# Performance work log

Hardware: AMD Instinct MI355X
Metric: run time of the kernel (lower is better)

Reference implementation:

```python
import jax, jax.numpy as jnp
import numpy as np

N_NODES = 50000
N_EDGES = 800000
DIM = 512
N_CLASSES = 1000


def _xavier(key, shape):
    fan_in, fan_out = shape[0], shape[1]
    lim = float(np.sqrt(6.0 / (fan_in + fan_out)))
    return jax.random.uniform(key, shape, jnp.float32, -lim, lim)


def setup_inputs() -> dict:
    key = jax.random.key(0)
    ks = jax.random.split(key, 12)
    nodes = jax.random.normal(ks[0], (N_NODES, DIM), jnp.float32)
    edges = jax.random.randint(ks[1], (2, N_EDGES), 0, N_NODES, jnp.int64)
    labelmatrix = jax.random.normal(ks[2], (N_CLASSES, 128), jnp.float32)
    return {
        "nodes": nodes,
        "edges": edges,
        "labelmatrix": labelmatrix,
        "W1": _xavier(ks[3], (DIM, 256)), "b1": jnp.zeros((256,), jnp.float32),
        "W2": _xavier(ks[4], (256, 192)), "b2": jnp.zeros((192,), jnp.float32),
        "W3": _xavier(ks[5], (192, 128)), "b3": jnp.zeros((128,), jnp.float32),
        "fc1_w": _xavier(ks[6], (128, 128)), "fc1_b": jnp.zeros((128,), jnp.float32),
        "fc2_w": _xavier(ks[7], (128, 128)), "fc2_b": jnp.zeros((128,), jnp.float32),
    }


def _gcn_conv(x, W, b, src, dst, n):
    # PyG GCNConv: add self-loops, symmetric normalization, then aggregate.
    xw = x @ W                                        # [N, out]
    ones = jnp.ones(src.shape[0], x.dtype)
    deg = jax.ops.segment_sum(ones, dst, num_segments=n) + 1.0  # +1 self-loop
    dinv = jax.lax.rsqrt(deg)                         # deg^{-1/2}
    coef = dinv[src] * dinv[dst]                      # [E]
    agg = jax.ops.segment_sum(xw[src] * coef[:, None], dst, num_segments=n)
    agg = agg + xw * (dinv * dinv)[:, None]           # self-loop contribution
    return agg + b


def reference(nodes, edges, labelmatrix, W1, b1, W2, b2, W3, b3,
              fc1_w, fc1_b, fc2_w, fc2_b):
    src, dst = edges[0], edges[1]
    n = nodes.shape[0]
    # _GraphConv: three stacked GCNConv layers, no inter-layer activation
    x = _gcn_conv(nodes, W1, b1, src, dst, n)
    x = _gcn_conv(x, W2, b2, src, dst, n)
    x = _gcn_conv(x, W3, b3, src, dst, n)             # [N, 128]
    # _GraphLinear (eval mode: dropout is identity)
    h = jax.nn.relu(x @ fc1_w + fc1_b)
    h = h @ fc2_w + fc2_b                             # [N, 128]
    preds = h @ labelmatrix.T                         # dot-product similarity [N, C]
    return preds
```

## Files before the change

kernel.cpp:

```cpp
#include <hip/hip_runtime.h>

typedef unsigned short u16;
typedef __bf16 bf16x8 __attribute__((ext_vector_type(8)));
typedef float f32x4 __attribute__((ext_vector_type(4)));

__device__ __forceinline__ u16 f2bf(float f) {
    unsigned int u = __float_as_uint(f);
    unsigned int r = (u + 0x7FFFu + ((u >> 16) & 1u)) >> 16;
    return (u16)r;
}
__device__ __forceinline__ float bf_lo(unsigned int u) { return __uint_as_float(u << 16); }
__device__ __forceinline__ float bf_hi(unsigned int u) { return __uint_as_float(u & 0xFFFF0000u); }

#define GLOAD_LDS(gp, lp) \
    __builtin_amdgcn_global_load_lds( \
        (const __attribute__((address_space(1))) unsigned int*)(gp), \
        (__attribute__((address_space(3))) unsigned int*)(lp), 16, 0, 0)


__global__ void hist_k(const int* __restrict__ dst, int* __restrict__ deg, int nE) {
    int e = blockIdx.x * 256 + threadIdx.x;
    if (e < nE) atomicAdd(&deg[dst[e]], 1);
}

__global__ void scan_block_k(const int* __restrict__ deg, int* __restrict__ scanned,
                             int* __restrict__ bsums, int n) {
    __shared__ int s[1024];
    int i = blockIdx.x * 1024 + threadIdx.x;
    int v = (i < n) ? deg[i] : 0;
    s[threadIdx.x] = v;
    __syncthreads();
    for (int off = 1; off < 1024; off <<= 1) {
        int t = (threadIdx.x >= off) ? s[threadIdx.x - off] : 0;
        __syncthreads();
        s[threadIdx.x] += t;
        __syncthreads();
    }
    if (i < n) scanned[i] = s[threadIdx.x];
    if (threadIdx.x == 1023) bsums[blockIdx.x] = s[1023];
}

__global__ void scan_sums_k(int* __restrict__ bsums, int nb) {
    int l = threadIdx.x & 63;
    int v = (l < nb) ? bsums[l] : 0;
    int orig = v;
    for (int off = 1; off < 64; off <<= 1) {
        int t = __shfl_up(v, off);
        if (l >= off) v += t;
    }
    if (l < nb) bsums[l] = v - orig;
}

__global__ void scan_final_dinv_k(const int* __restrict__ scanned, const int* __restrict__ deg,
                                  const int* __restrict__ bsums, int* __restrict__ rowptr,
                                  int* __restrict__ wptr, float* __restrict__ dinv,
                                  int n, int nE) {
    int i = blockIdx.x * 256 + threadIdx.x;
    if (i < n) {
        int rp = scanned[i] - deg[i] + bsums[i >> 10];
        rowptr[i] = rp;
        wptr[i] = rp;
        dinv[i] = rsqrtf((float)deg[i] + 1.0f);
    }
    if (i == 0) rowptr[n] = nE;
}

__global__ void csr_fill_k(const int* __restrict__ src, const int* __restrict__ dst,
                           int* __restrict__ wptr, const float* __restrict__ dinv,
                           int* __restrict__ eidx, float* __restrict__ ecoef, int nE) {
    int e = blockIdx.x * 256 + threadIdx.x;
    if (e >= nE) return;
    int d = dst[e], s = src[e];
    int p = atomicAdd(&wptr[d], 1);
    eidx[p] = s;
    ecoef[p] = dinv[s] * dinv[d];
}

__global__ void uv1_k(const int* __restrict__ rowptr, const float* __restrict__ ecoef,
                      const float* __restrict__ dinv, float* __restrict__ u1, int n) {
    int i = blockIdx.x * 256 + threadIdx.x;
    if (i >= n) return;
    float s = dinv[i] * dinv[i];
    int b = rowptr[i], e = rowptr[i + 1];
    for (int k = b; k < e; ++k) s += ecoef[k];
    u1[i] = s;
}

__global__ void uv2_k(const int* __restrict__ rowptr, const int* __restrict__ eidx,
                      const float* __restrict__ ecoef, const float* __restrict__ dinv,
                      const float* __restrict__ u1, float* __restrict__ u2, int n) {
    int i = blockIdx.x * 256 + threadIdx.x;
    if (i >= n) return;
    float s = dinv[i] * dinv[i] * u1[i];
    int b = rowptr[i], e = rowptr[i + 1];
    for (int k = b; k < e; ++k) s += ecoef[k] * u1[eidx[k]];
    u2[i] = s;
}


__global__ __launch_bounds__(192) void ck1_k(const float* __restrict__ W1,
                                             const float* __restrict__ W2,
                                             float* __restrict__ T1) {
    __shared__ float row[256];
    int i = blockIdx.x;
    for (int t = threadIdx.x; t < 256; t += 192) row[t] = W1[i * 256 + t];
    __syncthreads();
    int j = threadIdx.x;
    float s = 0.f;
    for (int k = 0; k < 256; ++k) s = fmaf(row[k], W2[k * 192 + j], s);
    T1[i * 192 + j] = s;
}

__global__ __launch_bounds__(128) void ck2_k(const float* __restrict__ T1,
                                             const float* __restrict__ W3,
                                             u16* __restrict__ Wp) {
    __shared__ float row[192];
    int i = blockIdx.x;
    for (int t = threadIdx.x; t < 192; t += 128) row[t] = T1[i * 192 + t];
    __syncthreads();
    int j = threadIdx.x;
    float s = 0.f;
    for (int m = 0; m < 192; ++m) s = fmaf(row[m], W3[m * 128 + j], s);
    Wp[(size_t)j * 512 + i] = f2bf(s);
}

__global__ __launch_bounds__(192) void ckvec_k(const float* __restrict__ b1, const float* __restrict__ W2,
                                               const float* __restrict__ b2, const float* __restrict__ W3,
                                               float* __restrict__ c1, float* __restrict__ c2) {
    __shared__ float t1b[192];
    int t = threadIdx.x;
    float s = 0.f;
    for (int k = 0; k < 256; ++k) s = fmaf(b1[k], W2[k * 192 + t], s);
    t1b[t] = s;
    __syncthreads();
    if (t < 128) {
        float a = 0.f, b = 0.f;
        for (int m = 0; m < 192; ++m) {
            a = fmaf(t1b[m], W3[m * 128 + t], a);
            b = fmaf(b2[m], W3[m * 128 + t], b);
        }
        c1[t] = a; c2[t] = b;
    }
}

__global__ void prepfc1_k(const float* __restrict__ Wf1, u16* __restrict__ Bf1) {
    int idx = blockIdx.x * 256 + threadIdx.x;
    if (idx >= 128 * 128) return;
    int nn = idx >> 7, k = idx & 127;
    Bf1[idx] = f2bf(Wf1[k * 128 + nn]);
}

__global__ __launch_bounds__(128) void fuse_fc2_k(
    const float* __restrict__ fc2_w, const float* __restrict__ fc2_b,
    const float* __restrict__ labelm, u16* __restrict__ Wc, float* __restrict__ bc) {
    __shared__ float w[128 * 129];
    __shared__ float lm[128];
    __shared__ float red[2];
    const int tid = threadIdx.x;
    for (int t = tid; t < 128 * 128; t += 128)
        w[(t >> 7) * 129 + (t & 127)] = fc2_w[t];
    __syncthreads();
    for (int cc = 0; cc < 8; ++cc) {
        int c = blockIdx.x * 8 + cc;
        lm[tid] = (c < 1000) ? labelm[(size_t)c * 128 + tid] : 0.f;
        __syncthreads();
        float sum = 0.f;
        const float* wr = &w[tid * 129];
        for (int j = 0; j < 128; ++j) sum = fmaf(wr[j], lm[j], sum);
        Wc[(size_t)c * 128 + tid] = f2bf(sum);
        float p = fc2_b[tid] * lm[tid];
        for (int off = 32; off > 0; off >>= 1) p += __shfl_down(p, off);
        if ((tid & 63) == 0) red[tid >> 6] = p;
        __syncthreads();
        if (tid == 0) bc[c] = red[0] + red[1];
        __syncthreads();
    }
}


template <bool CASTA, bool OUTF32, bool BIAS, bool RELU>
__global__ __launch_bounds__(256) void gemm_mfma(
    const void* __restrict__ Ap, const u16* __restrict__ Bt,
    const float* __restrict__ bias, void* __restrict__ Cout,
    int K, int Nout, int ldc, int Mout, int lgny, int Arows) {
    __shared__ __align__(16) u16 As[128 * 64];
    __shared__ __align__(16) u16 Bs[128 * 64];
    const int tid  = threadIdx.x;
    const int lane = tid & 63;
    const int w    = tid >> 6;
    const int wm   = w >> 1, wn = w & 1;

    const int nwg = gridDim.x, orig = blockIdx.x;
    const int q = nwg >> 3, r = nwg & 7;
    const int xcd = orig & 7, off = orig >> 3;
    const int tile = (xcd < r ? xcd * (q + 1) : r * (q + 1) + (xcd - r) * q) + off;
    const int ny = 1 << lgny;
    const int tx = tile >> lgny, ty = tile & (ny - 1);
    const size_t bm = (size_t)tx * 128;
    const size_t bn = (size_t)ty * 128;

    const int l7 = lane & 7;
    const int l3 = lane >> 3;
    const int kcs = l7 ^ l3;

    f32x4 acc[4][4] = {};

    for (int k0 = 0; k0 < K; k0 += 64) {
        if constexpr (CASTA) {
            const float* Af = (const float*)Ap;
            const int row = tid >> 1;
            const int half = tid & 1;
            const size_t grow = bm + row;
            const bool valid = grow < (size_t)Arows;
            const float4* g4 = (const float4*)(Af + grow * K + k0 + half * 32);
            float4 f[8];
#pragma unroll
            for (int j = 0; j < 8; ++j)
                f[j] = valid ? g4[j] : make_float4(0.f, 0.f, 0.f, 0.f);
#pragma unroll
            for (int j = 0; j < 4; ++j) {
                int kc = (half * 4 + j) ^ (row & 7);
                uint4 o;
                o.x = (unsigned)f2bf(f[2 * j].x)     | ((unsigned)f2bf(f[2 * j].y) << 16);
                o.y = (unsigned)f2bf(f[2 * j].z)     | ((unsigned)f2bf(f[2 * j].w) << 16);
                o.z = (unsigned)f2bf(f[2 * j + 1].x) | ((unsigned)f2bf(f[2 * j + 1].y) << 16);
                o.w = (unsigned)f2bf(f[2 * j + 1].z) | ((unsigned)f2bf(f[2 * j + 1].w) << 16);
                *(uint4*)((char*)As + row * 128 + kc * 16) = o;
            }
#pragma unroll
            for (int it = 0; it < 4; ++it) {
                const int r0 = w * 32 + it * 8;
                const u16* gB = Bt + ((size_t)(bn + r0 + l3) * K + k0) + kcs * 8;
                GLOAD_LDS(gB, Bs + r0 * 64);
            }
        } else {
            const u16* A = (const u16*)Ap;
#pragma unroll
            for (int it = 0; it < 4; ++it) {
                const int r0 = w * 32 + it * 8;
                const u16* gA = A + ((size_t)(bm + r0 + l3) * K + k0) + kcs * 8;
                GLOAD_LDS(gA, As + r0 * 64);
                const u16* gB = Bt + ((size_t)(bn + r0 + l3) * K + k0) + kcs * 8;
                GLOAD_LDS(gB, Bs + r0 * 64);
            }
        }
        __syncthreads();

#pragma unroll
        for (int ks = 0; ks < 2; ++ks) {
            bf16x8 av[4], bv[4];
#pragma unroll
            for (int i = 0; i < 4; ++i) {
                int row = wm * 64 + i * 16 + (lane & 15);
                int kc = (ks * 4 + (lane >> 4)) ^ (lane & 7);
                av[i] = *(const bf16x8*)((const char*)As + row * 128 + kc * 16);
            }
#pragma unroll
            for (int j = 0; j < 4; ++j) {
                int nn = wn * 64 + j * 16 + (lane & 15);
                int kc = (ks * 4 + (lane >> 4)) ^ (lane & 7);
                bv[j] = *(const bf16x8*)((const char*)Bs + nn * 128 + kc * 16);
            }
#pragma unroll
            for (int i = 0; i < 4; ++i)
#pragma unroll
                for (int j = 0; j < 4; ++j)
                    acc[i][j] = __builtin_amdgcn_mfma_f32_16x16x32_bf16(av[i], bv[j], acc[i][j], 0, 0, 0);
        }
        __syncthreads();
    }

    const int ccol  = lane & 15;
    const int crow4 = (lane >> 4) * 4;
#pragma unroll
    for (int i = 0; i < 4; ++i) {
#pragma unroll
        for (int j = 0; j < 4; ++j) {
#pragma unroll
            for (int r2 = 0; r2 < 4; ++r2) {
                size_t gr = bm + wm * 64 + i * 16 + crow4 + r2;
                size_t gc = bn + wn * 64 + j * 16 + ccol;
                if (gr < (size_t)Mout && gc < (size_t)Nout) {
                    float v = acc[i][j][r2];
                    if constexpr (BIAS) v += bias[gc];
                    if constexpr (RELU) v = fmaxf(v, 0.f);
                    if constexpr (OUTF32) ((float*)Cout)[gr * ldc + gc] = v;
                    else                  ((u16*)Cout)[gr * ldc + gc] = f2bf(v);
                }
            }
        }
    }
}


template <bool FINAL>
__global__ __launch_bounds__(256) void agg128_k(
    const u16* __restrict__ xw, const int* __restrict__ rowptr,
    const int* __restrict__ eidx, const float* __restrict__ ecoef,
    const float* __restrict__ dinv, u16* __restrict__ out,
    const float* __restrict__ u1v, const float* __restrict__ u2v,
    const float* __restrict__ c1, const float* __restrict__ c2,
    const float* __restrict__ b3, int n) {
    const int tid = threadIdx.x;
    const int sub = tid >> 4;
    const int fl  = tid & 15;
    int node = blockIdx.x * 16 + sub;
    if (node >= n) return;

    const uint4* xv = (const uint4*)xw;
    float di = dinv[node];
    float s = di * di;
    uint4 a = xv[(size_t)node * 16 + fl];
    float acc[8];
    acc[0] = s * bf_lo(a.x); acc[1] = s * bf_hi(a.x);
    acc[2] = s * bf_lo(a.y); acc[3] = s * bf_hi(a.y);
    acc[4] = s * bf_lo(a.z); acc[5] = s * bf_hi(a.z);
    acc[6] = s * bf_lo(a.w); acc[7] = s * bf_hi(a.w);

    int beg = rowptr[node], end = rowptr[node + 1];
    int e = beg;
    for (; e + 3 < end; e += 4) {
        int sn0 = eidx[e], sn1 = eidx[e + 1], sn2 = eidx[e + 2], sn3 = eidx[e + 3];
        float c0 = ecoef[e], cc1 = ecoef[e + 1], cc2 = ecoef[e + 2], c3 = ecoef[e + 3];
        uint4 v0 = xv[(size_t)sn0 * 16 + fl];
        uint4 v1 = xv[(size_t)sn1 * 16 + fl];
        uint4 v2 = xv[(size_t)sn2 * 16 + fl];
        uint4 v3 = xv[(size_t)sn3 * 16 + fl];
        acc[0] = fmaf(c0, bf_lo(v0.x), acc[0]); acc[1] = fmaf(c0, bf_hi(v0.x), acc[1]);
        acc[2] = fmaf(c0, bf_lo(v0.y), acc[2]); acc[3] = fmaf(c0, bf_hi(v0.y), acc[3]);
        acc[4] = fmaf(c0, bf_lo(v0.z), acc[4]); acc[5] = fmaf(c0, bf_hi(v0.z), acc[5]);
        acc[6] = fmaf(c0, bf_lo(v0.w), acc[6]); acc[7] = fmaf(c0, bf_hi(v0.w), acc[7]);
        acc[0] = fmaf(cc1, bf_lo(v1.x), acc[0]); acc[1] = fmaf(cc1, bf_hi(v1.x), acc[1]);
        acc[2] = fmaf(cc1, bf_lo(v1.y), acc[2]); acc[3] = fmaf(cc1, bf_hi(v1.y), acc[3]);
        acc[4] = fmaf(cc1, bf_lo(v1.z), acc[4]); acc[5] = fmaf(cc1, bf_hi(v1.z), acc[5]);
        acc[6] = fmaf(cc1, bf_lo(v1.w), acc[6]); acc[7] = fmaf(cc1, bf_hi(v1.w), acc[7]);
        acc[0] = fmaf(cc2, bf_lo(v2.x), acc[0]); acc[1] = fmaf(cc2, bf_hi(v2.x), acc[1]);
        acc[2] = fmaf(cc2, bf_lo(v2.y), acc[2]); acc[3] = fmaf(cc2, bf_hi(v2.y), acc[3]);
        acc[4] = fmaf(cc2, bf_lo(v2.z), acc[4]); acc[5] = fmaf(cc2, bf_hi(v2.z), acc[5]);
        acc[6] = fmaf(cc2, bf_lo(v2.w), acc[6]); acc[7] = fmaf(cc2, bf_hi(v2.w), acc[7]);
        acc[0] = fmaf(c3, bf_lo(v3.x), acc[0]); acc[1] = fmaf(c3, bf_hi(v3.x), acc[1]);
        acc[2] = fmaf(c3, bf_lo(v3.y), acc[2]); acc[3] = fmaf(c3, bf_hi(v3.y), acc[3]);
        acc[4] = fmaf(c3, bf_lo(v3.z), acc[4]); acc[5] = fmaf(c3, bf_hi(v3.z), acc[5]);
        acc[6] = fmaf(c3, bf_lo(v3.w), acc[6]); acc[7] = fmaf(c3, bf_hi(v3.w), acc[7]);
    }
    for (; e < end; ++e) {
        int sn = eidx[e];
        float c = ecoef[e];
        uint4 v = xv[(size_t)sn * 16 + fl];
        acc[0] = fmaf(c, bf_lo(v.x), acc[0]); acc[1] = fmaf(c, bf_hi(v.x), acc[1]);
        acc[2] = fmaf(c, bf_lo(v.y), acc[2]); acc[3] = fmaf(c, bf_hi(v.y), acc[3]);
        acc[4] = fmaf(c, bf_lo(v.z), acc[4]); acc[5] = fmaf(c, bf_hi(v.z), acc[5]);
        acc[6] = fmaf(c, bf_lo(v.w), acc[6]); acc[7] = fmaf(c, bf_hi(v.w), acc[7]);
    }

    if constexpr (FINAL) {
        float uu1 = u1v[node], uu2 = u2v[node];
        float4 c1a = ((const float4*)c1)[fl * 2], c1b = ((const float4*)c1)[fl * 2 + 1];
        float4 c2a = ((const float4*)c2)[fl * 2], c2b = ((const float4*)c2)[fl * 2 + 1];
        float4 b3a = ((const float4*)b3)[fl * 2], b3b = ((const float4*)b3)[fl * 2 + 1];
        acc[0] += uu2 * c1a.x + uu1 * c2a.x + b3a.x;
        acc[1] += uu2 * c1a.y + uu1 * c2a.y + b3a.y;
        acc[2] += uu2 * c1a.z + uu1 * c2a.z + b3a.z;
        acc[3] += uu2 * c1a.w + uu1 * c2a.w + b3a.w;
        acc[4] += uu2 * c1b.x + uu1 * c2b.x + b3b.x;
        acc[5] += uu2 * c1b.y + uu1 * c2b.y + b3b.y;
        acc[6] += uu2 * c1b.z + uu1 * c2b.z + b3b.z;
        acc[7] += uu2 * c1b.w + uu1 * c2b.w + b3b.w;
    }

    uint4 o;
    o.x = (unsigned)f2bf(acc[0]) | ((unsigned)f2bf(acc[1]) << 16);
    o.y = (unsigned)f2bf(acc[2]) | ((unsigned)f2bf(acc[3]) << 16);
    o.z = (unsigned)f2bf(acc[4]) | ((unsigned)f2bf(acc[5]) << 16);
    o.w = (unsigned)f2bf(acc[6]) | ((unsigned)f2bf(acc[7]) << 16);
    ((uint4*)out)[(size_t)node * 16 + fl] = o;
}


extern "C" void kernel_launch(void* const* d_in, const int* in_sizes, int n_in,
                              void* d_out, int out_size, void* d_ws, size_t ws_size,
                              hipStream_t stream) {
    const float* nodes  = (const float*)d_in[0];
    const int*   edges  = (const int*)d_in[1];
    const float* labelm = (const float*)d_in[2];
    const float* W1 = (const float*)d_in[3];
    const float* b1 = (const float*)d_in[4];
    const float* W2 = (const float*)d_in[5];
    const float* b2 = (const float*)d_in[6];
    const float* W3 = (const float*)d_in[7];
    const float* b3 = (const float*)d_in[8];
    const float* fc1_w = (const float*)d_in[9];
    const float* fc1_b = (const float*)d_in[10];
    const float* fc2_w = (const float*)d_in[11];
    const float* fc2_b = (const float*)d_in[12];
    float* out = (float*)d_out;

    const int DIM = 512, N3 = 128, NC = 1000;
    const int n  = in_sizes[0] / DIM;
    const int nE = in_sizes[1] / 2;
    const int Mpad = 50048;
    const int* src = edges;
    const int* dst = edges + nE;

    u16* Y = (u16*)((char*)d_out + 67108864);
    u16* Z = (u16*)((char*)d_out + 100663296);

    char* ws = (char*)d_ws;
    u16*   Q      = (u16*)(ws);
    u16*   Rb     = (u16*)(ws + 12812288);
    float* T1     = (float*)(ws + 25624576);
    u16*   Wp     = (u16*)(ws + 26017792);
    u16*   Bfc1   = (u16*)(ws + 26148864);
    u16*   Wc     = (u16*)(ws + 26181632);
    float* bc     = (float*)(ws + 26443776);
    float* c1     = (float*)(ws + 26447872);
    float* c2     = (float*)(ws + 26448384);
    float* u1     = (float*)(ws + 26448896);
    float* u2     = (float*)(ws + 26648896);
    int*   deg_i  = (int*)(ws + 26848896);
    float* dinv   = (float*)(ws + 27048896);
    int*   rowptr = (int*)(ws + 27248896);
    int*   wptr   = (int*)(ws + 27448960);
    int*   scanned= (int*)(ws + 27648960);
    int*   bsums  = (int*)(ws + 27848960);
    int*   eidx   = (int*)(ws + 27849216);
    float* ecoef  = (float*)(ws + 31049216);

    hipMemsetAsync(deg_i, 0, (size_t)n * 4, stream);
    hist_k<<<(nE + 255) / 256, 256, 0, stream>>>(dst, deg_i, nE);
    int nb = (n + 1023) / 1024;
    scan_block_k<<<nb, 1024, 0, stream>>>(deg_i, scanned, bsums, n);
    scan_sums_k<<<1, 64, 0, stream>>>(bsums, nb);
    scan_final_dinv_k<<<(n + 255) / 256, 256, 0, stream>>>(scanned, deg_i, bsums, rowptr, wptr, dinv, n, nE);
    csr_fill_k<<<(nE + 255) / 256, 256, 0, stream>>>(src, dst, wptr, dinv, eidx, ecoef, nE);
    uv1_k<<<(n + 255) / 256, 256, 0, stream>>>(rowptr, ecoef, dinv, u1, n);
    uv2_k<<<(n + 255) / 256, 256, 0, stream>>>(rowptr, eidx, ecoef, dinv, u1, u2, n);

    ck1_k<<<512, 192, 0, stream>>>(W1, W2, T1);
    ck2_k<<<512, 128, 0, stream>>>(T1, W3, Wp);
    ckvec_k<<<1, 192, 0, stream>>>(b1, W2, b2, W3, c1, c2);
    prepfc1_k<<<64, 256, 0, stream>>>(fc1_w, Bfc1);
    fuse_fc2_k<<<128, 128, 0, stream>>>(fc2_w, fc2_b, labelm, Wc, bc);

    const int gx = Mpad / 128;
    dim3 blk(256);
    const int gagg = (n + 15) / 16;

    gemm_mfma<true, false, false, false><<<gx, blk, 0, stream>>>(nodes, Wp, nullptr, Y, 512, N3, N3, Mpad, 0, n);
    agg128_k<false><<<gagg, blk, 0, stream>>>(Y, rowptr, eidx, ecoef, dinv, Z, nullptr, nullptr, nullptr, nullptr, nullptr, n);
    agg128_k<false><<<gagg, blk, 0, stream>>>(Z, rowptr, eidx, ecoef, dinv, Y, nullptr, nullptr, nullptr, nullptr, nullptr, n);
    agg128_k<true ><<<gagg, blk, 0, stream>>>(Y, rowptr, eidx, ecoef, dinv, Rb, u1, u2, c1, c2, b3, n);
    gemm_mfma<false, false, true, true><<<gx, blk, 0, stream>>>(Rb, Bfc1, fc1_b, Q, 128, N3, N3, Mpad, 0, Mpad);
    gemm_mfma<false, true, true, false><<<gx * 8, blk, 0, stream>>>(Q, Wc, bc, out, 128, NC, NC, n, 3, Mpad);
}
```

Before: 391.9 us.

## Fuse three aggregation passes into one cooperative kernel with grid syncs

```diff
diff --git a/kernel.cpp b/kernel.cpp
--- a/kernel.cpp
+++ b/kernel.cpp
@@ -1,4 +1,7 @@
 #include <hip/hip_runtime.h>
+#include <hip/hip_cooperative_groups.h>
+
+namespace cg = cooperative_groups;
 
 typedef unsigned short u16;
 typedef __bf16 bf16x8 __attribute__((ext_vector_type(8)));
@@ -54,47 +57,31 @@
 __global__ void scan_final_dinv_k(const int* __restrict__ scanned, const int* __restrict__ deg,
                                   const int* __restrict__ bsums, int* __restrict__ rowptr,
                                   int* __restrict__ wptr, float* __restrict__ dinv,
-                                  int n, int nE) {
+                                  float* __restrict__ u1, int n, int nE) {
     int i = blockIdx.x * 256 + threadIdx.x;
     if (i < n) {
         int rp = scanned[i] - deg[i] + bsums[i >> 10];
         rowptr[i] = rp;
         wptr[i] = rp;
-        dinv[i] = rsqrtf((float)deg[i] + 1.0f);
+        float di = rsqrtf((float)deg[i] + 1.0f);
+        dinv[i] = di;
+        u1[i] = di * di;
     }
     if (i == 0) rowptr[n] = nE;
 }
 
 __global__ void csr_fill_k(const int* __restrict__ src, const int* __restrict__ dst,
                            int* __restrict__ wptr, const float* __restrict__ dinv,
-                           int* __restrict__ eidx, float* __restrict__ ecoef, int nE) {
+                           int* __restrict__ eidx, float* __restrict__ ecoef,
+                           float* __restrict__ u1, int nE) {
     int e = blockIdx.x * 256 + threadIdx.x;
     if (e >= nE) return;
     int d = dst[e], s = src[e];
     int p = atomicAdd(&wptr[d], 1);
+    float c = dinv[s] * dinv[d];
     eidx[p] = s;
-    ecoef[p] = dinv[s] * dinv[d];
-}
-
-__global__ void uv1_k(const int* __restrict__ rowptr, const float* __restrict__ ecoef,
-                      const float* __restrict__ dinv, float* __restrict__ u1, int n) {
-    int i = blockIdx.x * 256 + threadIdx.x;
-    if (i >= n) return;
-    float s = dinv[i] * dinv[i];
-    int b = rowptr[i], e = rowptr[i + 1];
-    for (int k = b; k < e; ++k) s += ecoef[k];
-    u1[i] = s;
-}
-
-__global__ void uv2_k(const int* __restrict__ rowptr, const int* __restrict__ eidx,
-                      const float* __restrict__ ecoef, const float* __restrict__ dinv,
-                      const float* __restrict__ u1, float* __restrict__ u2, int n) {
-    int i = blockIdx.x * 256 + threadIdx.x;
-    if (i >= n) return;
-    float s = dinv[i] * dinv[i] * u1[i];
-    int b = rowptr[i], e = rowptr[i + 1];
-    for (int k = b; k < e; ++k) s += ecoef[k] * u1[eidx[k]];
-    u2[i] = s;
+    ecoef[p] = c;
+    atomicAdd(&u1[d], c);
 }
 
 
@@ -111,43 +98,43 @@
     T1[i * 192 + j] = s;
 }
 
-__global__ __launch_bounds__(128) void ck2_k(const float* __restrict__ T1,
-                                             const float* __restrict__ W3,
-                                             u16* __restrict__ Wp) {
-    __shared__ float row[192];
-    int i = blockIdx.x;
-    for (int t = threadIdx.x; t < 192; t += 128) row[t] = T1[i * 192 + t];
-    __syncthreads();
-    int j = threadIdx.x;
-    float s = 0.f;
-    for (int m = 0; m < 192; ++m) s = fmaf(row[m], W3[m * 128 + j], s);
-    Wp[(size_t)j * 512 + i] = f2bf(s);
-}
-
-__global__ __launch_bounds__(192) void ckvec_k(const float* __restrict__ b1, const float* __restrict__ W2,
-                                               const float* __restrict__ b2, const float* __restrict__ W3,
-                                               float* __restrict__ c1, float* __restrict__ c2) {
-    __shared__ float t1b[192];
-    int t = threadIdx.x;
-    float s = 0.f;
-    for (int k = 0; k < 256; ++k) s = fmaf(b1[k], W2[k * 192 + t], s);
-    t1b[t] = s;
-    __syncthreads();
-    if (t < 128) {
-        float a = 0.f, b = 0.f;
-        for (int m = 0; m < 192; ++m) {
-            a = fmaf(t1b[m], W3[m * 128 + t], a);
-            b = fmaf(b2[m], W3[m * 128 + t], b);
-        }
-        c1[t] = a; c2[t] = b;
-    }
-}
-
-__global__ void prepfc1_k(const float* __restrict__ Wf1, u16* __restrict__ Bf1) {
-    int idx = blockIdx.x * 256 + threadIdx.x;
-    if (idx >= 128 * 128) return;
-    int nn = idx >> 7, k = idx & 127;
-    Bf1[idx] = f2bf(Wf1[k * 128 + nn]);
+__global__ __launch_bounds__(256) void prep2_k(
+    const float* __restrict__ T1, const float* __restrict__ W3, u16* __restrict__ Wp,
+    const float* __restrict__ b1, const float* __restrict__ W2, const float* __restrict__ b2,
+    float* __restrict__ c1, float* __restrict__ c2,
+    const float* __restrict__ fc1_w, u16* __restrict__ Bfc1) {
+    __shared__ float sbuf[192];
+    const int b = blockIdx.x, tid = threadIdx.x;
+    if (b < 512) {
+        if (tid < 192) sbuf[tid] = T1[b * 192 + tid];
+        __syncthreads();
+        if (tid < 128) {
+            float s = 0.f;
+            for (int m = 0; m < 192; ++m) s = fmaf(sbuf[m], W3[m * 128 + tid], s);
+            Wp[(size_t)tid * 512 + b] = f2bf(s);
+        }
+    } else if (b == 512) {
+        if (tid < 192) {
+            float s = 0.f;
+            for (int k = 0; k < 256; ++k) s = fmaf(b1[k], W2[k * 192 + tid], s);
+            sbuf[tid] = s;
+        }
+        __syncthreads();
+        if (tid < 128) {
+            float a = 0.f, bb = 0.f;
+            for (int m = 0; m < 192; ++m) {
+                a  = fmaf(sbuf[m], W3[m * 128 + tid], a);
+                bb = fmaf(b2[m],   W3[m * 128 + tid], bb);
+            }
+            c1[tid] = a; c2[tid] = bb;
+        }
+    } else {
+        int idx = (b - 513) * 256 + tid;
+        if (idx < 128 * 128) {
+            int nn = idx >> 7, k = idx & 127;
+            Bfc1[idx] = f2bf(fc1_w[k * 128 + nn]);
+        }
+    }
 }
 
 __global__ __launch_bounds__(128) void fuse_fc2_k(
@@ -294,86 +281,110 @@
 
 
 template <bool FINAL>
-__global__ __launch_bounds__(256) void agg128_k(
-    const u16* __restrict__ xw, const int* __restrict__ rowptr,
-    const int* __restrict__ eidx, const float* __restrict__ ecoef,
-    const float* __restrict__ dinv, u16* __restrict__ out,
+__device__ __forceinline__ void agg_pass(
+    const u16* __restrict__ xw, u16* __restrict__ out,
+    const int* __restrict__ rowptr, const int* __restrict__ eidx,
+    const float* __restrict__ ecoef, const float* __restrict__ dinv,
     const float* __restrict__ u1v, const float* __restrict__ u2v,
     const float* __restrict__ c1, const float* __restrict__ c2,
-    const float* __restrict__ b3, int n) {
+    const float* __restrict__ b3, int n, int ngrp) {
     const int tid = threadIdx.x;
     const int sub = tid >> 4;
     const int fl  = tid & 15;
-    int node = blockIdx.x * 16 + sub;
-    if (node >= n) return;
-
     const uint4* xv = (const uint4*)xw;
-    float di = dinv[node];
-    float s = di * di;
-    uint4 a = xv[(size_t)node * 16 + fl];
-    float acc[8];
-    acc[0] = s * bf_lo(a.x); acc[1] = s * bf_hi(a.x);
-    acc[2] = s * bf_lo(a.y); acc[3] = s * bf_hi(a.y);
-    acc[4] = s * bf_lo(a.z); acc[5] = s * bf_hi(a.z);
-    acc[6] = s * bf_lo(a.w); acc[7] = s * bf_hi(a.w);
-
-    int beg = rowptr[node], end = rowptr[node + 1];
-    int e = beg;
-    for (; e + 3 < end; e += 4) {
-        int sn0 = eidx[e], sn1 = eidx[e + 1], sn2 = eidx[e + 2], sn3 = eidx[e + 3];
-        float c0 = ecoef[e], cc1 = ecoef[e + 1], cc2 = ecoef[e + 2], c3 = ecoef[e + 3];
-        uint4 v0 = xv[(size_t)sn0 * 16 + fl];
-        uint4 v1 = xv[(size_t)sn1 * 16 + fl];
-        uint4 v2 = xv[(size_t)sn2 * 16 + fl];
-        uint4 v3 = xv[(size_t)sn3 * 16 + fl];
-        acc[0] = fmaf(c0, bf_lo(v0.x), acc[0]); acc[1] = fmaf(c0, bf_hi(v0.x), acc[1]);
-        acc[2] = fmaf(c0, bf_lo(v0.y), acc[2]); acc[3] = fmaf(c0, bf_hi(v0.y), acc[3]);
-        acc[4] = fmaf(c0, bf_lo(v0.z), acc[4]); acc[5] = fmaf(c0, bf_hi(v0.z), acc[5]);
-        acc[6] = fmaf(c0, bf_lo(v0.w), acc[6]); acc[7] = fmaf(c0, bf_hi(v0.w), acc[7]);
-        acc[0] = fmaf(cc1, bf_lo(v1.x), acc[0]); acc[1] = fmaf(cc1, bf_hi(v1.x), acc[1]);
-        acc[2] = fmaf(cc1, bf_lo(v1.y), acc[2]); acc[3] = fmaf(cc1, bf_hi(v1.y), acc[3]);
-        acc[4] = fmaf(cc1, bf_lo(v1.z), acc[4]); acc[5] = fmaf(cc1, bf_hi(v1.z), acc[5]);
-        acc[6] = fmaf(cc1, bf_lo(v1.w), acc[6]); acc[7] = fmaf(cc1, bf_hi(v1.w), acc[7]);
-        acc[0] = fmaf(cc2, bf_lo(v2.x), acc[0]); acc[1] = fmaf(cc2, bf_hi(v2.x), acc[1]);
-        acc[2] = fmaf(cc2, bf_lo(v2.y), acc[2]); acc[3] = fmaf(cc2, bf_hi(v2.y), acc[3]);
-        acc[4] = fmaf(cc2, bf_lo(v2.z), acc[4]); acc[5] = fmaf(cc2, bf_hi(v2.z), acc[5]);
-        acc[6] = fmaf(cc2, bf_lo(v2.w), acc[6]); acc[7] = fmaf(cc2, bf_hi(v2.w), acc[7]);
-        acc[0] = fmaf(c3, bf_lo(v3.x), acc[0]); acc[1] = fmaf(c3, bf_hi(v3.x), acc[1]);
-        acc[2] = fmaf(c3, bf_lo(v3.y), acc[2]); acc[3] = fmaf(c3, bf_hi(v3.y), acc[3]);
-        acc[4] = fmaf(c3, bf_lo(v3.z), acc[4]); acc[5] = fmaf(c3, bf_hi(v3.z), acc[5]);
-        acc[6] = fmaf(c3, bf_lo(v3.w), acc[6]); acc[7] = fmaf(c3, bf_hi(v3.w), acc[7]);
-    }
-    for (; e < end; ++e) {
-        int sn = eidx[e];
-        float c = ecoef[e];
-        uint4 v = xv[(size_t)sn * 16 + fl];
-        acc[0] = fmaf(c, bf_lo(v.x), acc[0]); acc[1] = fmaf(c, bf_hi(v.x), acc[1]);
-        acc[2] = fmaf(c, bf_lo(v.y), acc[2]); acc[3] = fmaf(c, bf_hi(v.y), acc[3]);
-        acc[4] = fmaf(c, bf_lo(v.z), acc[4]); acc[5] = fmaf(c, bf_hi(v.z), acc[5]);
-        acc[6] = fmaf(c, bf_lo(v.w), acc[6]); acc[7] = fmaf(c, bf_hi(v.w), acc[7]);
-    }
-
-    if constexpr (FINAL) {
-        float uu1 = u1v[node], uu2 = u2v[node];
-        float4 c1a = ((const float4*)c1)[fl * 2], c1b = ((const float4*)c1)[fl * 2 + 1];
-        float4 c2a = ((const float4*)c2)[fl * 2], c2b = ((const float4*)c2)[fl * 2 + 1];
-        float4 b3a = ((const float4*)b3)[fl * 2], b3b = ((const float4*)b3)[fl * 2 + 1];
-        acc[0] += uu2 * c1a.x + uu1 * c2a.x + b3a.x;
-        acc[1] += uu2 * c1a.y + uu1 * c2a.y + b3a.y;
-        acc[2] += uu2 * c1a.z + uu1 * c2a.z + b3a.z;
-        acc[3] += uu2 * c1a.w + uu1 * c2a.w + b3a.w;
-        acc[4] += uu2 * c1b.x + uu1 * c2b.x + b3b.x;
-        acc[5] += uu2 * c1b.y + uu1 * c2b.y + b3b.y;
-        acc[6] += uu2 * c1b.z + uu1 * c2b.z + b3b.z;
-        acc[7] += uu2 * c1b.w + uu1 * c2b.w + b3b.w;
-    }
-
-    uint4 o;
-    o.x = (unsigned)f2bf(acc[0]) | ((unsigned)f2bf(acc[1]) << 16);
-    o.y = (unsigned)f2bf(acc[2]) | ((unsigned)f2bf(acc[3]) << 16);
-    o.z = (unsigned)f2bf(acc[4]) | ((unsigned)f2bf(acc[5]) << 16);
-    o.w = (unsigned)f2bf(acc[6]) | ((unsigned)f2bf(acc[7]) << 16);
-    ((uint4*)out)[(size_t)node * 16 + fl] = o;
+    for (int g = blockIdx.x; g < ngrp; g += gridDim.x) {
+        int node = g * 16 + sub;
+        if (node >= n) continue;
+        float di = dinv[node];
+        float s = di * di;
+        uint4 a = xv[(size_t)node * 16 + fl];
+        float acc[8];
+        acc[0] = s * bf_lo(a.x); acc[1] = s * bf_hi(a.x);
+        acc[2] = s * bf_lo(a.y); acc[3] = s * bf_hi(a.y);
+        acc[4] = s * bf_lo(a.z); acc[5] = s * bf_hi(a.z);
+        acc[6] = s * bf_lo(a.w); acc[7] = s * bf_hi(a.w);
+
+        int beg = rowptr[node], end = rowptr[node + 1];
+        int e = beg;
+        for (; e + 3 < end; e += 4) {
+            int sn0 = eidx[e], sn1 = eidx[e + 1], sn2 = eidx[e + 2], sn3 = eidx[e + 3];
+            float c0 = ecoef[e], cx1 = ecoef[e + 1], cx2 = ecoef[e + 2], c3 = ecoef[e + 3];
+            uint4 v0 = xv[(size_t)sn0 * 16 + fl];
+            uint4 v1 = xv[(size_t)sn1 * 16 + fl];
+            uint4 v2 = xv[(size_t)sn2 * 16 + fl];
+            uint4 v3 = xv[(size_t)sn3 * 16 + fl];
+            acc[0] = fmaf(c0, bf_lo(v0.x), acc[0]); acc[1] = fmaf(c0, bf_hi(v0.x), acc[1]);
+            acc[2] = fmaf(c0, bf_lo(v0.y), acc[2]); acc[3] = fmaf(c0, bf_hi(v0.y), acc[3]);
+            acc[4] = fmaf(c0, bf_lo(v0.z), acc[4]); acc[5] = fmaf(c0, bf_hi(v0.z), acc[5]);
+            acc[6] = fmaf(c0, bf_lo(v0.w), acc[6]); acc[7] = fmaf(c0, bf_hi(v0.w), acc[7]);
+            acc[0] = fmaf(cx1, bf_lo(v1.x), acc[0]); acc[1] = fmaf(cx1, bf_hi(v1.x), acc[1]);
+            acc[2] = fmaf(cx1, bf_lo(v1.y), acc[2]); acc[3] = fmaf(cx1, bf_hi(v1.y), acc[3]);
+            acc[4] = fmaf(cx1, bf_lo(v1.z), acc[4]); acc[5] = fmaf(cx1, bf_hi(v1.z), acc[5]);
+            acc[6] = fmaf(cx1, bf_lo(v1.w), acc[6]); acc[7] = fmaf(cx1, bf_hi(v1.w), acc[7]);
+            acc[0] = fmaf(cx2, bf_lo(v2.x), acc[0]); acc[1] = fmaf(cx2, bf_hi(v2.x), acc[1]);
+            acc[2] = fmaf(cx2, bf_lo(v2.y), acc[2]); acc[3] = fmaf(cx2, bf_hi(v2.y), acc[3]);
+            acc[4] = fmaf(cx2, bf_lo(v2.z), acc[4]); acc[5] = fmaf(cx2, bf_hi(v2.z), acc[5]);
+            acc[6] = fmaf(cx2, bf_lo(v2.w), acc[6]); acc[7] = fmaf(cx2, bf_hi(v2.w), acc[7]);
+            acc[0] = fmaf(c3, bf_lo(v3.x), acc[0]); acc[1] = fmaf(c3, bf_hi(v3.x), acc[1]);
+            acc[2] = fmaf(c3, bf_lo(v3.y), acc[2]); acc[3] = fmaf(c3, bf_hi(v3.y), acc[3]);
+            acc[4] = fmaf(c3, bf_lo(v3.z), acc[4]); acc[5] = fmaf(c3, bf_hi(v3.z), acc[5]);
+            acc[6] = fmaf(c3, bf_lo(v3.w), acc[6]); acc[7] = fmaf(c3, bf_hi(v3.w), acc[7]);
+        }
+        for (; e < end; ++e) {
+            int sn = eidx[e];
+            float c = ecoef[e];
+            uint4 v = xv[(size_t)sn * 16 + fl];
+            acc[0] = fmaf(c, bf_lo(v.x), acc[0]); acc[1] = fmaf(c, bf_hi(v.x), acc[1]);
+            acc[2] = fmaf(c, bf_lo(v.y), acc[2]); acc[3] = fmaf(c, bf_hi(v.y), acc[3]);
+            acc[4] = fmaf(c, bf_lo(v.z), acc[4]); acc[5] = fmaf(c, bf_hi(v.z), acc[5]);
+            acc[6] = fmaf(c, bf_lo(v.w), acc[6]); acc[7] = fmaf(c, bf_hi(v.w), acc[7]);
+        }
+
+        if constexpr (FINAL) {
+            float uu1 = u1v[node], uu2 = u2v[node];
+            float4 c1a = ((const float4*)c1)[fl * 2], c1b = ((const float4*)c1)[fl * 2 + 1];
+            float4 c2a = ((const float4*)c2)[fl * 2], c2b = ((const float4*)c2)[fl * 2 + 1];
+            float4 b3a = ((const float4*)b3)[fl * 2], b3b = ((const float4*)b3)[fl * 2 + 1];
+            acc[0] += uu2 * c1a.x + uu1 * c2a.x + b3a.x;
+            acc[1] += uu2 * c1a.y + uu1 * c2a.y + b3a.y;
+            acc[2] += uu2 * c1a.z + uu1 * c2a.z + b3a.z;
+            acc[3] += uu2 * c1a.w + uu1 * c2a.w + b3a.w;
+            acc[4] += uu2 * c1b.x + uu1 * c2b.x + b3b.x;
+            acc[5] += uu2 * c1b.y + uu1 * c2b.y + b3b.y;
+            acc[6] += uu2 * c1b.z + uu1 * c2b.z + b3b.z;
+            acc[7] += uu2 * c1b.w + uu1 * c2b.w + b3b.w;
+        }
+
+        uint4 o;
+        o.x = (unsigned)f2bf(acc[0]) | ((unsigned)f2bf(acc[1]) << 16);
+        o.y = (unsigned)f2bf(acc[2]) | ((unsigned)f2bf(acc[3]) << 16);
+        o.z = (unsigned)f2bf(acc[4]) | ((unsigned)f2bf(acc[5]) << 16);
+        o.w = (unsigned)f2bf(acc[6]) | ((unsigned)f2bf(acc[7]) << 16);
+        ((uint4*)out)[(size_t)node * 16 + fl] = o;
+    }
+}
+
+__global__ __launch_bounds__(256, 4) void agg3_k(
+    u16* __restrict__ Y, u16* __restrict__ Z, u16* __restrict__ Rb,
+    const int* __restrict__ rowptr, const int* __restrict__ eidx,
+    const float* __restrict__ ecoef, const float* __restrict__ dinv,
+    const float* __restrict__ u1, float* __restrict__ u2,
+    const float* __restrict__ c1, const float* __restrict__ c2,
+    const float* __restrict__ b3, int n, int ngrp) {
+    cg::grid_group grid = cg::this_grid();
+    for (int i = blockIdx.x * 256 + threadIdx.x; i < n; i += gridDim.x * 256) {
+        float s = dinv[i] * dinv[i] * u1[i];
+        int b = rowptr[i], e = rowptr[i + 1];
+        for (int k = b; k < e; ++k) s += ecoef[k] * u1[eidx[k]];
+        u2[i] = s;
+    }
+    agg_pass<false>(Y, Z, rowptr, eidx, ecoef, dinv, nullptr, nullptr, nullptr, nullptr, nullptr, n, ngrp);
+    __threadfence();
+    grid.sync();
+    agg_pass<false>(Z, Y, rowptr, eidx, ecoef, dinv, nullptr, nullptr, nullptr, nullptr, nullptr, n, ngrp);
+    __threadfence();
+    grid.sync();
+    agg_pass<true>(Y, Rb, rowptr, eidx, ecoef, dinv, u1, u2, c1, c2, b3, n, ngrp);
 }
 
 
@@ -431,25 +442,30 @@
     int nb = (n + 1023) / 1024;
     scan_block_k<<<nb, 1024, 0, stream>>>(deg_i, scanned, bsums, n);
     scan_sums_k<<<1, 64, 0, stream>>>(bsums, nb);
-    scan_final_dinv_k<<<(n + 255) / 256, 256, 0, stream>>>(scanned, deg_i, bsums, rowptr, wptr, dinv, n, nE);
-    csr_fill_k<<<(nE + 255) / 256, 256, 0, stream>>>(src, dst, wptr, dinv, eidx, ecoef, nE);
-    uv1_k<<<(n + 255) / 256, 256, 0, stream>>>(rowptr, ecoef, dinv, u1, n);
-    uv2_k<<<(n + 255) / 256, 256, 0, stream>>>(rowptr, eidx, ecoef, dinv, u1, u2, n);
+    scan_final_dinv_k<<<(n + 255) / 256, 256, 0, stream>>>(scanned, deg_i, bsums, rowptr, wptr, dinv, u1, n, nE);
+    csr_fill_k<<<(nE + 255) / 256, 256, 0, stream>>>(src, dst, wptr, dinv, eidx, ecoef, u1, nE);
 
     ck1_k<<<512, 192, 0, stream>>>(W1, W2, T1);
-    ck2_k<<<512, 128, 0, stream>>>(T1, W3, Wp);
-    ckvec_k<<<1, 192, 0, stream>>>(b1, W2, b2, W3, c1, c2);
-    prepfc1_k<<<64, 256, 0, stream>>>(fc1_w, Bfc1);
+    prep2_k<<<577, 256, 0, stream>>>(T1, W3, Wp, b1, W2, b2, c1, c2, fc1_w, Bfc1);
     fuse_fc2_k<<<128, 128, 0, stream>>>(fc2_w, fc2_b, labelm, Wc, bc);
 
     const int gx = Mpad / 128;
     dim3 blk(256);
-    const int gagg = (n + 15) / 16;
 
     gemm_mfma<true, false, false, false><<<gx, blk, 0, stream>>>(nodes, Wp, nullptr, Y, 512, N3, N3, Mpad, 0, n);
-    agg128_k<false><<<gagg, blk, 0, stream>>>(Y, rowptr, eidx, ecoef, dinv, Z, nullptr, nullptr, nullptr, nullptr, nullptr, n);
-    agg128_k<false><<<gagg, blk, 0, stream>>>(Z, rowptr, eidx, ecoef, dinv, Y, nullptr, nullptr, nullptr, nullptr, nullptr, n);
-    agg128_k<true ><<<gagg, blk, 0, stream>>>(Y, rowptr, eidx, ecoef, dinv, Rb, u1, u2, c1, c2, b3, n);
+
+    {
+        int ngrp = (n + 15) / 16;
+        int n_ = n;
+        u16 *Yp = Y, *Zp = Z, *Rp = Rb;
+        const int* rp = rowptr; const int* ei = eidx;
+        const float *ec = ecoef, *dv = dinv, *u1p = u1, *c1p = c1, *c2p = c2, *b3p = b3;
+        float* u2p = u2;
+        void* cargs[] = {&Yp, &Zp, &Rp, (void*)&rp, (void*)&ei, (void*)&ec, (void*)&dv,
+                         (void*)&u1p, &u2p, (void*)&c1p, (void*)&c2p, (void*)&b3p, &n_, &ngrp};
+        hipLaunchCooperativeKernel((void*)agg3_k, dim3(1024), dim3(256), cargs, 0, stream);
+    }
+
     gemm_mfma<false, false, true, true><<<gx, blk, 0, stream>>>(Rb, Bfc1, fc1_b, Q, 128, N3, N3, Mpad, 0, Mpad);
     gemm_mfma<false, true, true, false><<<gx * 8, blk, 0, stream>>>(Q, Wc, bc, out, 128, NC, NC, n, 3, Mpad);
 }
```

Result: slower. 891.8 us (+127.6%).
